# Optimization experiments

Measured on AMD Instinct MI355X. Metric: run time of the kernel, lower is better.

Reference implementation:

```python
import jax, jax.numpy as jnp
import numpy as np

B, N, C = 2, 4096, 512
H = 8
K = 512  # num pivotal tokens


def setup_inputs() -> dict:
    key = jax.random.key(0)
    k1, k2, k3 = jax.random.split(key, 3)
    x = jax.random.normal(k1, (B, N, C), dtype=jnp.float32)
    w_qkv = jax.random.normal(k2, (C, 3 * C), dtype=jnp.float32) * (C ** -0.5)
    w_proj = jax.random.normal(k3, (C, C), dtype=jnp.float32) * (C ** -0.5)
    b_proj = jnp.zeros((C,), dtype=jnp.float32)
    return {"x": x, "w_qkv": w_qkv, "w_proj": w_proj, "b_proj": b_proj,
            "num_heads": H, "num_pivots": K}


def reference(x, w_qkv, w_proj, b_proj, num_heads, num_pivots):
    b, n, c = x.shape
    h = num_heads
    d = c // h
    scale = d ** -0.5
    # qkv projection -> q, k, v each [b, h, n, d]
    qkv = (x @ w_qkv).reshape(b, n, 3, h, d)
    q, k, v = jnp.moveaxis(qkv, 2, 0)          # each [b, n, h, d]
    q = jnp.swapaxes(q, 1, 2)                  # [b, h, n, d]
    k = jnp.swapaxes(k, 1, 2)
    v = jnp.swapaxes(v, 1, 2)
    # raw attention scores, materialized (the custom-kernel hotspot)
    attn = jax.nn.softmax(jnp.einsum('bhqd,bhkd->bhqk', q, k) * scale, axis=-1)
    # standard attention output + projection
    out = jnp.einsum('bhqk,bhkd->bhqd', attn, v)       # [b, h, n, d]
    out = jnp.swapaxes(out, 1, 2).reshape(b, n, c)     # [b, n, c]
    out = out @ w_proj + b_proj
    # pivotal-token importance: attention mass each token receives,
    # averaged over heads and queries -> [b, n]
    importance = attn.mean(axis=1).mean(axis=1)
    _, idx = jax.lax.top_k(importance, num_pivots)     # [b, K]
    # gather pivotal tokens -> reduced sequence [b, K, c]
    pivots = jnp.take_along_axis(out, idx[:, :, None], axis=1)
    return pivots
```

## Files before the change

kernel.cpp:

```cpp
#include <hip/hip_runtime.h>
#include <hip/hip_bf16.h>

#define BB 2
#define NN 4096
#define CC 512
#define HH 8
#define DD 64
#define KPIV 512
#define SCALE 0.125f
#define C2INV 4.8828125e-4f
#define C2    2048.0f

typedef unsigned short ushort_t;
typedef __attribute__((ext_vector_type(8))) short short8;
typedef __attribute__((ext_vector_type(8))) _Float16 half8;
typedef __attribute__((ext_vector_type(16))) float float16;

__device__ __forceinline__ float bf2f(ushort_t h) {
    union { unsigned u; float f; } x; x.u = ((unsigned)h) << 16; return x.f;
}
__device__ __forceinline__ ushort_t f2bf(float f) {
    __hip_bfloat16 h = __float2bfloat16(f);
    ushort_t u;
    __builtin_memcpy(&u, &h, sizeof(u));
    return u;
}
__device__ __forceinline__ void split2h(float x, _Float16& hi, _Float16& lo) {
    hi = (_Float16)x;
    lo = (_Float16)((x - (float)hi) * C2);
}

#define COLP(c) ((((c) >> 3) * 12) + ((c) & 7))
#define ROWSTR 196

__global__ __launch_bounds__(256) void qkv_gemm_k(
    const float* __restrict__ x, const float* __restrict__ w,
    _Float16* __restrict__ qhg, _Float16* __restrict__ qlg,
    _Float16* __restrict__ khg, _Float16* __restrict__ klg,
    ushort_t* __restrict__ vt)
{
    __shared__ __attribute__((aligned(16))) float xs[16 * ROWSTR];
    __shared__ __attribute__((aligned(16))) float ws[16 * ROWSTR];
    const int t = threadIdx.x;
    const int row0 = blockIdx.x * 128;
    const int col0 = blockIdx.y * 128;
    const int tr = t & 15, tc = t >> 4;
    const int ts = col0 >> 9;
    float acc[8][8] = {};
    for (int k0 = 0; k0 < CC; k0 += 16) {
        __syncthreads();
        {
            const int r = t >> 1, off = (t & 1) * 8;
            const float* xp = x + (size_t)(row0 + r) * CC + k0 + off;
            float4 v0 = *(const float4*)xp;
            float4 v1 = *(const float4*)(xp + 4);
            float xv[8] = {v0.x, v0.y, v0.z, v0.w, v1.x, v1.y, v1.z, v1.w};
            const int mc = COLP(r);
            #pragma unroll
            for (int jj = 0; jj < 8; ++jj)
                xs[(off + jj) * ROWSTR + mc] = xv[jj];
        }
        {
            const int kk = t >> 4, c8 = (t & 15) * 8;
            const float* wp2 = w + (size_t)(k0 + kk) * (3 * CC) + col0 + c8;
            const int nc = kk * ROWSTR + COLP(c8);
            *(float4*)&ws[nc]     = *(const float4*)wp2;
            *(float4*)&ws[nc + 4] = *(const float4*)(wp2 + 4);
        }
        __syncthreads();
        #pragma unroll
        for (int kk = 0; kk < 16; ++kk) {
            float a[8], b[8];
            const int ab = kk * ROWSTR + tr * 12;
            const int bb = kk * ROWSTR + tc * 12;
            *(float4*)&a[0] = *(const float4*)&xs[ab];
            *(float4*)&a[4] = *(const float4*)&xs[ab + 4];
            *(float4*)&b[0] = *(const float4*)&ws[bb];
            *(float4*)&b[4] = *(const float4*)&ws[bb + 4];
            #pragma unroll
            for (int i = 0; i < 8; ++i)
                #pragma unroll
                for (int j = 0; j < 8; ++j)
                    acc[i][j] = fmaf(a[i], b[j], acc[i][j]);
        }
    }
    const int gc0 = col0 + tc * 8;
    const int hh = (gc0 >> 6) & 7;
    const int dd0 = gc0 & 63;
    #pragma unroll
    for (int i = 0; i < 8; ++i) {
        const int grow = row0 + tr * 8 + i;
        const int b = grow >> 12, n = grow & (NN - 1);
        const size_t base = (((size_t)b * HH + hh) * NN + n) * DD + dd0;
        if (ts == 0) {
            half8 h8, l8;
            #pragma unroll
            for (int j = 0; j < 8; ++j) {
                _Float16 a2, b2; split2h(acc[i][j] * SCALE, a2, b2);
                h8[j] = a2; l8[j] = b2;
            }
            *(half8*)(qhg + base) = h8;
            *(half8*)(qlg + base) = l8;
        } else if (ts == 1) {
            half8 h8, l8;
            #pragma unroll
            for (int j = 0; j < 8; ++j) {
                _Float16 a2, b2; split2h(acc[i][j], a2, b2);
                h8[j] = a2; l8[j] = b2;
            }
            *(half8*)(khg + base) = h8;
            *(half8*)(klg + base) = l8;
        } else {
            #pragma unroll
            for (int j = 0; j < 8; ++j)
                vt[(((size_t)b * HH + hh) * DD + dd0 + j) * NN + n] = f2bf(acc[i][j]);
        }
    }
}

__device__ __forceinline__ void load_q_frags(
    const _Float16* __restrict__ qhg, const _Float16* __restrict__ qlg,
    size_t qrow, int g, half8* qh, half8* ql)
{
    const size_t off = qrow * DD + g * 8;
    #pragma unroll
    for (int kd = 0; kd < 4; ++kd) {
        qh[kd] = *(const half8*)(qhg + off + kd * 16);
        ql[kd] = *(const half8*)(qlg + off + kd * 16);
    }
}

__device__ __forceinline__ void stage_k128(
    const _Float16* __restrict__ khg, const _Float16* __restrict__ klg,
    int bh, int n0, int t, half8* khs, half8* kls)
{
    const _Float16* kb = khg + ((size_t)bh * NN + n0) * DD;
    const _Float16* lb = klg + ((size_t)bh * NN + n0) * DD;
    #pragma unroll
    for (int j = 0; j < 4; ++j) {
        const int s = t + j * 256;
        const int seg = s >> 7, tok = s & 127;
        const size_t off = (size_t)tok * DD + seg * 8;
        *(uint4*)&khs[seg * 128 + tok] = *(const uint4*)(kb + off);
        *(uint4*)&kls[seg * 128 + tok] = *(const uint4*)(lb + off);
    }
}

#define S_STEP_LDS(khs, kls, t0)                                              \
    float16 a0, a12;                                                          \
    _Pragma("unroll")                                                         \
    for (int i = 0; i < 16; ++i) { a0[i] = 0.f; a12[i] = 0.f; }               \
    _Pragma("unroll")                                                         \
    for (int kd = 0; kd < 4; ++kd) {                                          \
        half8 bh8 = (khs)[(kd * 2 + g) * 128 + (t0) + ln];                    \
        half8 bl8 = (kls)[(kd * 2 + g) * 128 + (t0) + ln];                    \
        a0  = __builtin_amdgcn_mfma_f32_32x32x16_f16(qh[kd], bh8, a0, 0,0,0); \
        a12 = __builtin_amdgcn_mfma_f32_32x32x16_f16(ql[kd], bh8, a12,0,0,0); \
        a12 = __builtin_amdgcn_mfma_f32_32x32x16_f16(qh[kd], bl8, a12,0,0,0); \
    }

#define S_STEP_G(koff)                                                         \
    float16 a0, a12;                                                           \
    _Pragma("unroll")                                                          \
    for (int i = 0; i < 16; ++i) { a0[i] = 0.f; a12[i] = 0.f; }                \
    _Pragma("unroll")                                                          \
    for (int kd = 0; kd < 4; ++kd) {                                           \
        half8 bh8 = *(const half8*)(khg + (koff) + kd * 16);                   \
        half8 bl8 = *(const half8*)(klg + (koff) + kd * 16);                   \
        a0  = __builtin_amdgcn_mfma_f32_32x32x16_f16(qh[kd], bh8, a0, 0,0,0);  \
        a12 = __builtin_amdgcn_mfma_f32_32x32x16_f16(ql[kd], bh8, a12,0,0,0);  \
        a12 = __builtin_amdgcn_mfma_f32_32x32x16_f16(qh[kd], bl8, a12,0,0,0);  \
    }

__global__ __launch_bounds__(256) void pass_a_k(
    const _Float16* __restrict__ qhg, const _Float16* __restrict__ qlg,
    const _Float16* __restrict__ khg, const _Float16* __restrict__ klg,
    float* __restrict__ l)
{
    __shared__ half8 khs[2][8 * 128];
    __shared__ half8 kls[2][8 * 128];
    const int t = threadIdx.x;
    const int lane = t & 63, wv = t >> 6;
    const int g = lane >> 5, ln = lane & 31;
    const int bh = blockIdx.x >> 5;
    const int qt = blockIdx.x & 31;
    half8 qh[4], ql[4];
    load_q_frags(qhg, qlg, (size_t)bh * NN + qt * 128 + wv * 32 + ln, g, qh, ql);
    float rowacc[16];
    #pragma unroll
    for (int r = 0; r < 16; ++r) rowacc[r] = 0.f;
    stage_k128(khg, klg, bh, 0, t, khs[0], kls[0]);
    __syncthreads();
    for (int ss = 0; ss < 32; ++ss) {
        if (ss + 1 < 32)
            stage_k128(khg, klg, bh, (ss + 1) * 128, t,
                       khs[(ss + 1) & 1], kls[(ss + 1) & 1]);
        const half8* kh = khs[ss & 1];
        const half8* kl = kls[ss & 1];
        #pragma unroll
        for (int ii = 0; ii < 4; ++ii) {
            S_STEP_LDS(kh, kl, ii * 32)
            #pragma unroll
            for (int r = 0; r < 16; ++r)
                rowacc[r] += __expf(fmaf(a12[r], C2INV, a0[r]));
        }
        __syncthreads();
    }
    #pragma unroll
    for (int r = 0; r < 16; ++r) {
        float vs = rowacc[r];
        vs += __shfl_xor(vs, 1);
        vs += __shfl_xor(vs, 2);
        vs += __shfl_xor(vs, 4);
        vs += __shfl_xor(vs, 8);
        vs += __shfl_xor(vs, 16);
        rowacc[r] = vs;
    }
    if (ln == 0) {
        #pragma unroll
        for (int r = 0; r < 16; ++r) {
            const int row = (r & 3) + 8 * (r >> 2) + 4 * g;
            l[(size_t)bh * NN + qt * 128 + wv * 32 + row] = rowacc[r];
        }
    }
}

__global__ __launch_bounds__(256) void pass_b_k(
    const _Float16* __restrict__ qhg, const _Float16* __restrict__ qlg,
    const _Float16* __restrict__ khg, const _Float16* __restrict__ klg,
    const float* __restrict__ l, float* __restrict__ colsum)
{
    __shared__ half8 khs[8 * 128];
    __shared__ half8 kls[8 * 128];
    __shared__ float colbuf[4][128];
    const int t = threadIdx.x;
    const int lane = t & 63, wv = t >> 6;
    const int g = lane >> 5, ln = lane & 31;
    const int bh = blockIdx.x >> 6;
    const int qt = (blockIdx.x >> 1) & 31;
    const int th = blockIdx.x & 1;
    const int rowout = blockIdx.x >> 1;
    const int base_n = th * 2048;
    half8 qh[4], ql[4];
    load_q_frags(qhg, qlg, (size_t)bh * NN + qt * 128 + wv * 32 + ln, g, qh, ql);
    float rv[16];
    #pragma unroll
    for (int r = 0; r < 16; ++r) {
        const int row = (r & 3) + 8 * (r >> 2) + 4 * g;
        rv[r] = 1.0f / l[(size_t)bh * NN + qt * 128 + wv * 32 + row];
    }
    for (int ss = 0; ss < 16; ++ss) {
        __syncthreads();
        if (ss > 0 && t < 128)
            colsum[(size_t)rowout * NN + base_n + (ss - 1) * 128 + t] =
                (colbuf[0][t] + colbuf[1][t]) + (colbuf[2][t] + colbuf[3][t]);
        stage_k128(khg, klg, bh, base_n + ss * 128, t, khs, kls);
        __syncthreads();
        #pragma unroll
        for (int ii = 0; ii < 4; ++ii) {
            S_STEP_LDS(khs, kls, ii * 32)
            float cs = 0.f;
            #pragma unroll
            for (int r = 0; r < 16; ++r)
                cs = fmaf(__expf(fmaf(a12[r], C2INV, a0[r])), rv[r], cs);
            cs += __shfl_xor(cs, 32);
            if (g == 0) colbuf[wv][ii * 32 + ln] = cs;
        }
    }
    __syncthreads();
    if (t < 128)
        colsum[(size_t)rowout * NN + base_n + 2048 - 128 + t] =
            (colbuf[0][t] + colbuf[1][t]) + (colbuf[2][t] + colbuf[3][t]);
}

__global__ __launch_bounds__(256) void imp_reduce_k(
    const float* __restrict__ colsum, double* __restrict__ imp)
{
    const int n = blockIdx.x * 256 + threadIdx.x;
    const int b = n >> 12, c = n & (NN - 1);
    const float* p = colsum + (size_t)b * 256 * NN + c;
    double s = 0.0;
    for (int i = 0; i < 256; ++i) s += (double)p[(size_t)i * NN];
    imp[n] = s * (1.0 / (double)(HH * NN));
}

__global__ __launch_bounds__(1024) void topk_k(
    const double* __restrict__ imp, int* __restrict__ idxout)
{
    __shared__ double sv[4096];
    __shared__ int si[4096];
    const int b = blockIdx.x, t = threadIdx.x;
    for (int i = t; i < 4096; i += 1024) { sv[i] = imp[b * 4096 + i]; si[i] = i; }
    __syncthreads();
    for (int kk = 2; kk <= 4096; kk <<= 1) {
        for (int j = kk >> 1; j > 0; j >>= 1) {
            #pragma unroll 1
            for (int r = 0; r < 2; ++r) {
                const int cm = t + r * 1024;
                const int i = ((cm & ~(j - 1)) << 1) | (cm & (j - 1));
                const int lo = i | j;
                const bool up = ((i & kk) == 0);
                const double va = sv[i], vb = sv[lo];
                const int ia = si[i], ib = si[lo];
                const bool after = (va < vb) || (va == vb && ia > ib);
                if (after == up) { sv[i] = vb; sv[lo] = va; si[i] = ib; si[lo] = ia; }
            }
            __syncthreads();
        }
    }
    if (t < KPIV) idxout[b * KPIV + t] = si[t];
}

__global__ __launch_bounds__(256) void pass_c_k(
    const _Float16* __restrict__ qhg, const _Float16* __restrict__ qlg,
    const _Float16* __restrict__ khg, const _Float16* __restrict__ klg,
    const ushort_t* __restrict__ vt, const float* __restrict__ l,
    const int* __restrict__ idx, float* __restrict__ opiv)
{
    __shared__ short8 pfr[4][4][32];
    __shared__ __attribute__((aligned(16))) float osum[4][32][64];
    const int t = threadIdx.x;
    const int lane = t & 63, wv = t >> 6;
    const int g = lane >> 5, ln = lane & 31;
    const int bid = blockIdx.x;
    const int b = bid >> 8, h = (bid >> 5) & 7;
    const int chunk = (bid >> 1) & 15, th = bid & 1;
    const int bh = b * HH + h;
    const int r0 = chunk * 32;
    const int tokq = idx[b * KPIV + r0 + ln];
    half8 qh[4], ql[4];
    load_q_frags(qhg, qlg, (size_t)bh * NN + tokq, g, qh, ql);
    float rv[16];
    #pragma unroll
    for (int r = 0; r < 16; ++r) {
        const int row = (r & 3) + 8 * (r >> 2) + 4 * g;
        rv[r] = 1.0f / l[(size_t)bh * NN + idx[b * KPIV + r0 + row]];
    }
    float16 oacc0, oacc1;
    #pragma unroll
    for (int i = 0; i < 16; ++i) { oacc0[i] = 0.f; oacc1[i] = 0.f; }
    const int base_n = th * 2048 + wv * 512;
    for (int step = 0; step < 16; ++step) {
        const int n0 = base_n + step * 32;
        const size_t koff = ((size_t)bh * NN + n0 + ln) * DD + g * 8;
        S_STEP_G(koff)
        __syncthreads();
        #pragma unroll
        for (int r = 0; r < 16; ++r) {
            const int row = (r & 3) + 8 * (r >> 2) + 4 * g;
            const float p = __expf(fmaf(a12[r], C2INV, a0[r])) * rv[r];
            *((ushort_t*)&pfr[wv][ln >> 3][row] + (ln & 7)) = f2bf(p);
        }
        __syncthreads();
        #pragma unroll
        for (int kh2 = 0; kh2 < 2; ++kh2) {
            short8 pa = pfr[wv][kh2 * 2 + g][ln];
            const ushort_t* vp0 = vt + ((size_t)bh * DD + ln) * NN + n0 + kh2 * 16 + g * 8;
            uint4 u0 = *(const uint4*)vp0;
            uint4 u1 = *(const uint4*)(vp0 + (size_t)32 * NN);
            short8 vb0, vb1;
            __builtin_memcpy(&vb0, &u0, 16);
            __builtin_memcpy(&vb1, &u1, 16);
            oacc0 = __builtin_amdgcn_mfma_f32_32x32x16_bf16(pa, vb0, oacc0, 0,0,0);
            oacc1 = __builtin_amdgcn_mfma_f32_32x32x16_bf16(pa, vb1, oacc1, 0,0,0);
        }
    }
    #pragma unroll
    for (int r = 0; r < 16; ++r) {
        const int row = (r & 3) + 8 * (r >> 2) + 4 * g;
        osum[wv][row][ln]      = oacc0[r];
        osum[wv][row][32 + ln] = oacc1[r];
    }
    __syncthreads();
    {
        const int qrow = t >> 3, d0 = (t & 7) * 8;
        float s[8] = {};
        #pragma unroll
        for (int w = 0; w < 4; ++w) {
            float4 a  = *(const float4*)&osum[w][qrow][d0];
            float4 b2 = *(const float4*)&osum[w][qrow][d0 + 4];
            s[0] += a.x;  s[1] += a.y;  s[2] += a.z;  s[3] += a.w;
            s[4] += b2.x; s[5] += b2.y; s[6] += b2.z; s[7] += b2.w;
        }
        float* op = opiv + ((size_t)(b * KPIV + r0 + qrow)) * CC + h * DD + d0;
        #pragma unroll
        for (int j = 0; j < 8; ++j) atomicAdd(op + j, s[j]);
    }
}

__global__ __launch_bounds__(256) void proj_k(
    const float* __restrict__ opiv, const float* __restrict__ wp,
    const float* __restrict__ bp, float* __restrict__ out)
{
    __shared__ __attribute__((aligned(16))) float os[8][CC];
    const int t = threadIdx.x;
    const int r0 = blockIdx.x * 8;
    for (int f = t; f < 1024; f += 256) {
        const int rr = f >> 7, i = (f & 127) * 4;
        *(float4*)&os[rr][i] = *(const float4*)(opiv + (size_t)(r0 + rr) * CC + i);
    }
    __syncthreads();
    const int c0 = t;
    float acc0[8] = {}, acc1[8] = {};
    for (int i = 0; i < CC; ++i) {
        const float w0 = wp[(size_t)i * CC + c0];
        const float w1 = wp[(size_t)i * CC + c0 + 256];
        #pragma unroll
        for (int rr = 0; rr < 8; ++rr) {
            const float ov = os[rr][i];
            acc0[rr] = fmaf(ov, w0, acc0[rr]);
            acc1[rr] = fmaf(ov, w1, acc1[rr]);
        }
    }
    const float b0 = bp[c0], b1 = bp[c0 + 256];
    #pragma unroll
    for (int rr = 0; rr < 8; ++rr) {
        out[((size_t)(r0 + rr)) * CC + c0]       = acc0[rr] + b0;
        out[((size_t)(r0 + rr)) * CC + c0 + 256] = acc1[rr] + b1;
    }
}

extern "C" void kernel_launch(void* const* d_in, const int* in_sizes, int n_in,
                              void* d_out, int out_size, void* d_ws, size_t ws_size,
                              hipStream_t stream)
{
    const float* x     = (const float*)d_in[0];
    const float* wqkv  = (const float*)d_in[1];
    const float* wproj = (const float*)d_in[2];
    const float* bproj = (const float*)d_in[3];

    const size_t NE = (size_t)BB * HH * NN * DD;
    _Float16*  qhg    = (_Float16*)d_ws;
    _Float16*  qlg    = qhg + NE;
    _Float16*  khg    = qlg + NE;
    _Float16*  klg    = khg + NE;
    ushort_t*  v      = (ushort_t*)(klg + NE);
    float*     l      = (float*)(v + NE);
    float*     colsum = l + (size_t)BB * HH * NN;
    double*    imp    = (double*)(colsum + (size_t)512 * NN);
    int*       idx    = (int*)(imp + BB * NN);
    float*     opiv   = (float*)(idx + BB * KPIV);
    float*     out    = (float*)d_out;

    const size_t need = (size_t)((char*)(opiv + (size_t)BB * KPIV * CC) - (char*)d_ws);
    if (ws_size < need) return;

    qkv_gemm_k<<<dim3(64, 12), 256, 0, stream>>>(x, wqkv, qhg, qlg, khg, klg, v);
    pass_a_k<<<512, 256, 0, stream>>>(qhg, qlg, khg, klg, l);
    pass_b_k<<<1024, 256, 0, stream>>>(qhg, qlg, khg, klg, l, colsum);
    imp_reduce_k<<<32, 256, 0, stream>>>(colsum, imp);
    topk_k<<<2, 1024, 0, stream>>>(imp, idx);
    hipMemsetAsync(opiv, 0, (size_t)BB * KPIV * CC * sizeof(float), stream);
    pass_c_k<<<512, 256, 0, stream>>>(qhg, qlg, khg, klg, v, l, idx, opiv);
    proj_k<<<128, 256, 0, stream>>>(opiv, wproj, bproj, out);
}
```

Baseline: 668.3 us.

## Split softmax denominator pass across key halves, double-buffer QKV GEMM, widen proj grid

Pass A now splits the key range into two halves per query tile, doubling the block count to 1024. Each half writes a partial row-sum that the later passes add before taking the reciprocal. This also drops pass A's LDS double buffering in favour of single-buffered staging. Separately, the QKV GEMM gains double-buffered shared-memory staging with one barrier per k-step, and the projection kernel splits output columns across two blocks to double its grid. The aim is better GPU occupancy and latency hiding, at the cost of extra partial-sum storage and twice the shared memory in the GEMM.

```diff
diff --git a/kernel.cpp b/kernel.cpp
--- a/kernel.cpp
+++ b/kernel.cpp
@@ -10,6 +10,7 @@
 #define SCALE 0.125f
 #define C2INV 4.8828125e-4f
 #define C2    2048.0f
+#define NROWS 65536
 
 typedef unsigned short ushort_t;
 typedef __attribute__((ext_vector_type(8))) short short8;
@@ -39,16 +40,16 @@
     _Float16* __restrict__ khg, _Float16* __restrict__ klg,
     ushort_t* __restrict__ vt)
 {
-    __shared__ __attribute__((aligned(16))) float xs[16 * ROWSTR];
-    __shared__ __attribute__((aligned(16))) float ws[16 * ROWSTR];
+    __shared__ __attribute__((aligned(16))) float xs[2][16 * ROWSTR];
+    __shared__ __attribute__((aligned(16))) float ws[2][16 * ROWSTR];
     const int t = threadIdx.x;
     const int row0 = blockIdx.x * 128;
     const int col0 = blockIdx.y * 128;
     const int tr = t & 15, tc = t >> 4;
     const int ts = col0 >> 9;
     float acc[8][8] = {};
-    for (int k0 = 0; k0 < CC; k0 += 16) {
-        __syncthreads();
+
+    auto stage = [&](int k0, float* xsb, float* wsb) {
         {
             const int r = t >> 1, off = (t & 1) * 8;
             const float* xp = x + (size_t)(row0 + r) * CC + k0 + off;
@@ -58,31 +59,40 @@
             const int mc = COLP(r);
             #pragma unroll
             for (int jj = 0; jj < 8; ++jj)
-                xs[(off + jj) * ROWSTR + mc] = xv[jj];
+                xsb[(off + jj) * ROWSTR + mc] = xv[jj];
         }
         {
             const int kk = t >> 4, c8 = (t & 15) * 8;
             const float* wp2 = w + (size_t)(k0 + kk) * (3 * CC) + col0 + c8;
             const int nc = kk * ROWSTR + COLP(c8);
-            *(float4*)&ws[nc]     = *(const float4*)wp2;
-            *(float4*)&ws[nc + 4] = *(const float4*)(wp2 + 4);
-        }
-        __syncthreads();
+            *(float4*)&wsb[nc]     = *(const float4*)wp2;
+            *(float4*)&wsb[nc + 4] = *(const float4*)(wp2 + 4);
+        }
+    };
+
+    stage(0, xs[0], ws[0]);
+    __syncthreads();
+    for (int it = 0; it < 32; ++it) {
+        if (it + 1 < 32)
+            stage((it + 1) * 16, xs[(it + 1) & 1], ws[(it + 1) & 1]);
+        const float* xsb = xs[it & 1];
+        const float* wsb = ws[it & 1];
         #pragma unroll
         for (int kk = 0; kk < 16; ++kk) {
             float a[8], b[8];
             const int ab = kk * ROWSTR + tr * 12;
             const int bb = kk * ROWSTR + tc * 12;
-            *(float4*)&a[0] = *(const float4*)&xs[ab];
-            *(float4*)&a[4] = *(const float4*)&xs[ab + 4];
-            *(float4*)&b[0] = *(const float4*)&ws[bb];
-            *(float4*)&b[4] = *(const float4*)&ws[bb + 4];
+            *(float4*)&a[0] = *(const float4*)&xsb[ab];
+            *(float4*)&a[4] = *(const float4*)&xsb[ab + 4];
+            *(float4*)&b[0] = *(const float4*)&wsb[bb];
+            *(float4*)&b[4] = *(const float4*)&wsb[bb + 4];
             #pragma unroll
             for (int i = 0; i < 8; ++i)
                 #pragma unroll
                 for (int j = 0; j < 8; ++j)
                     acc[i][j] = fmaf(a[i], b[j], acc[i][j]);
         }
+        __syncthreads();
     }
     const int gc0 = col0 + tc * 8;
     const int hh = (gc0 >> 6) & 7;
@@ -175,36 +185,33 @@
 __global__ __launch_bounds__(256) void pass_a_k(
     const _Float16* __restrict__ qhg, const _Float16* __restrict__ qlg,
     const _Float16* __restrict__ khg, const _Float16* __restrict__ klg,
-    float* __restrict__ l)
-{
-    __shared__ half8 khs[2][8 * 128];
-    __shared__ half8 kls[2][8 * 128];
+    float* __restrict__ lpart)
+{
+    __shared__ half8 khs[8 * 128];
+    __shared__ half8 kls[8 * 128];
     const int t = threadIdx.x;
     const int lane = t & 63, wv = t >> 6;
     const int g = lane >> 5, ln = lane & 31;
-    const int bh = blockIdx.x >> 5;
-    const int qt = blockIdx.x & 31;
+    const int bh = blockIdx.x >> 6;
+    const int qt = (blockIdx.x >> 1) & 31;
+    const int th = blockIdx.x & 1;
+    const int base_n = th * 2048;
     half8 qh[4], ql[4];
     load_q_frags(qhg, qlg, (size_t)bh * NN + qt * 128 + wv * 32 + ln, g, qh, ql);
     float rowacc[16];
     #pragma unroll
     for (int r = 0; r < 16; ++r) rowacc[r] = 0.f;
-    stage_k128(khg, klg, bh, 0, t, khs[0], kls[0]);
-    __syncthreads();
-    for (int ss = 0; ss < 32; ++ss) {
-        if (ss + 1 < 32)
-            stage_k128(khg, klg, bh, (ss + 1) * 128, t,
-                       khs[(ss + 1) & 1], kls[(ss + 1) & 1]);
-        const half8* kh = khs[ss & 1];
-        const half8* kl = kls[ss & 1];
+    for (int ss = 0; ss < 16; ++ss) {
+        __syncthreads();
+        stage_k128(khg, klg, bh, base_n + ss * 128, t, khs, kls);
+        __syncthreads();
         #pragma unroll
         for (int ii = 0; ii < 4; ++ii) {
-            S_STEP_LDS(kh, kl, ii * 32)
+            S_STEP_LDS(khs, kls, ii * 32)
             #pragma unroll
             for (int r = 0; r < 16; ++r)
                 rowacc[r] += __expf(fmaf(a12[r], C2INV, a0[r]));
         }
-        __syncthreads();
     }
     #pragma unroll
     for (int r = 0; r < 16; ++r) {
@@ -220,7 +227,8 @@
         #pragma unroll
         for (int r = 0; r < 16; ++r) {
             const int row = (r & 3) + 8 * (r >> 2) + 4 * g;
-            l[(size_t)bh * NN + qt * 128 + wv * 32 + row] = rowacc[r];
+            lpart[(size_t)th * NROWS + (size_t)bh * NN + qt * 128 + wv * 32 + row]
+                = rowacc[r];
         }
     }
 }
@@ -228,7 +236,7 @@
 __global__ __launch_bounds__(256) void pass_b_k(
     const _Float16* __restrict__ qhg, const _Float16* __restrict__ qlg,
     const _Float16* __restrict__ khg, const _Float16* __restrict__ klg,
-    const float* __restrict__ l, float* __restrict__ colsum)
+    const float* __restrict__ lpart, float* __restrict__ colsum)
 {
     __shared__ half8 khs[8 * 128];
     __shared__ half8 kls[8 * 128];
@@ -247,7 +255,8 @@
     #pragma unroll
     for (int r = 0; r < 16; ++r) {
         const int row = (r & 3) + 8 * (r >> 2) + 4 * g;
-        rv[r] = 1.0f / l[(size_t)bh * NN + qt * 128 + wv * 32 + row];
+        const size_t li = (size_t)bh * NN + qt * 128 + wv * 32 + row;
+        rv[r] = 1.0f / (lpart[li] + lpart[NROWS + li]);
     }
     for (int ss = 0; ss < 16; ++ss) {
         __syncthreads();
@@ -314,7 +323,7 @@
 __global__ __launch_bounds__(256) void pass_c_k(
     const _Float16* __restrict__ qhg, const _Float16* __restrict__ qlg,
     const _Float16* __restrict__ khg, const _Float16* __restrict__ klg,
-    const ushort_t* __restrict__ vt, const float* __restrict__ l,
+    const ushort_t* __restrict__ vt, const float* __restrict__ lpart,
     const int* __restrict__ idx, float* __restrict__ opiv)
 {
     __shared__ short8 pfr[4][4][32];
@@ -334,7 +343,8 @@
     #pragma unroll
     for (int r = 0; r < 16; ++r) {
         const int row = (r & 3) + 8 * (r >> 2) + 4 * g;
-        rv[r] = 1.0f / l[(size_t)bh * NN + idx[b * KPIV + r0 + row]];
+        const size_t li = (size_t)bh * NN + idx[b * KPIV + r0 + row];
+        rv[r] = 1.0f / (lpart[li] + lpart[NROWS + li]);
     }
     float16 oacc0, oacc1;
     #pragma unroll
@@ -394,30 +404,25 @@
 {
     __shared__ __attribute__((aligned(16))) float os[8][CC];
     const int t = threadIdx.x;
-    const int r0 = blockIdx.x * 8;
+    const int r0 = (blockIdx.x >> 1) * 8;
+    const int ch = blockIdx.x & 1;
     for (int f = t; f < 1024; f += 256) {
         const int rr = f >> 7, i = (f & 127) * 4;
         *(float4*)&os[rr][i] = *(const float4*)(opiv + (size_t)(r0 + rr) * CC + i);
     }
     __syncthreads();
-    const int c0 = t;
-    float acc0[8] = {}, acc1[8] = {};
+    const int c0 = ch * 256 + t;
+    float acc0[8] = {};
     for (int i = 0; i < CC; ++i) {
         const float w0 = wp[(size_t)i * CC + c0];
-        const float w1 = wp[(size_t)i * CC + c0 + 256];
-        #pragma unroll
-        for (int rr = 0; rr < 8; ++rr) {
-            const float ov = os[rr][i];
-            acc0[rr] = fmaf(ov, w0, acc0[rr]);
-            acc1[rr] = fmaf(ov, w1, acc1[rr]);
-        }
-    }
-    const float b0 = bp[c0], b1 = bp[c0 + 256];
-    #pragma unroll
-    for (int rr = 0; rr < 8; ++rr) {
-        out[((size_t)(r0 + rr)) * CC + c0]       = acc0[rr] + b0;
-        out[((size_t)(r0 + rr)) * CC + c0 + 256] = acc1[rr] + b1;
-    }
+        #pragma unroll
+        for (int rr = 0; rr < 8; ++rr)
+            acc0[rr] = fmaf(os[rr][i], w0, acc0[rr]);
+    }
+    const float b0 = bp[c0];
+    #pragma unroll
+    for (int rr = 0; rr < 8; ++rr)
+        out[((size_t)(r0 + rr)) * CC + c0] = acc0[rr] + b0;
 }
 
 extern "C" void kernel_launch(void* const* d_in, const int* in_sizes, int n_in,
@@ -435,8 +440,8 @@
     _Float16*  khg    = qlg + NE;
     _Float16*  klg    = khg + NE;
     ushort_t*  v      = (ushort_t*)(klg + NE);
-    float*     l      = (float*)(v + NE);
-    float*     colsum = l + (size_t)BB * HH * NN;
+    float*     lpart  = (float*)(v + NE);
+    float*     colsum = lpart + (size_t)2 * NROWS;
     double*    imp    = (double*)(colsum + (size_t)512 * NN);
     int*       idx    = (int*)(imp + BB * NN);
     float*     opiv   = (float*)(idx + BB * KPIV);
@@ -446,11 +451,11 @@
     if (ws_size < need) return;
 
     qkv_gemm_k<<<dim3(64, 12), 256, 0, stream>>>(x, wqkv, qhg, qlg, khg, klg, v);
-    pass_a_k<<<512, 256, 0, stream>>>(qhg, qlg, khg, klg, l);
-    pass_b_k<<<1024, 256, 0, stream>>>(qhg, qlg, khg, klg, l, colsum);
+    pass_a_k<<<1024, 256, 0, stream>>>(qhg, qlg, khg, klg, lpart);
+    pass_b_k<<<1024, 256, 0, stream>>>(qhg, qlg, khg, klg, lpart, colsum);
     imp_reduce_k<<<32, 256, 0, stream>>>(colsum, imp);
     topk_k<<<2, 1024, 0, stream>>>(imp, idx);
     hipMemsetAsync(opiv, 0, (size_t)BB * KPIV * CC * sizeof(float), stream);
-    pass_c_k<<<512, 256, 0, stream>>>(qhg, qlg, khg, klg, v, l, idx, opiv);
-    proj_k<<<128, 256, 0, stream>>>(opiv, wproj, bproj, out);
-}
+    pass_c_k<<<512, 256, 0, stream>>>(qhg, qlg, khg, klg, v, lpart, idx, opiv);
+    proj_k<<<256, 256, 0, stream>>>(opiv, wproj, bproj, out);
+}
```

After: 678.4 us. No clear change (+1.5%).
